# Kernel optimization log

Hardware: AMD Instinct MI355X
Metric: run time of the kernel (lower is better)

The kernel has to match this reference:

```python
import jax, jax.numpy as jnp
import numpy as np

MIN_R, MAX_R = -51.2, 51.2
ORIG_W, ORIG_H = 800.0, 448.0


def sample_bilinear(feat, gx, gy):
    # feat [N,C,H,W]; gx,gy [N,Q] in grid coords [-1,1], align_corners=True, zeros padding
    N, C, H, W = feat.shape
    px = (gx + 1.0) * 0.5 * (W - 1)
    py = (gy + 1.0) * 0.5 * (H - 1)
    x0 = jnp.floor(px)
    y0 = jnp.floor(py)
    x0i = x0.astype(jnp.int32)
    y0i = y0.astype(jnp.int32)
    wx1 = px - x0
    wy1 = py - y0
    ff = feat.reshape(N, C, H * W)

    def corner(xi, yi, w):
        valid = (xi >= 0) & (xi < W) & (yi >= 0) & (yi < H)
        idx = jnp.clip(yi, 0, H - 1) * W + jnp.clip(xi, 0, W - 1)
        vals = jax.vmap(lambda f, i: f[:, i])(ff, idx)  # [N,C,Q]
        return vals * (w * valid.astype(w.dtype))[:, None, :]

    return (corner(x0i, y0i, (1 - wx1) * (1 - wy1))
            + corner(x0i + 1, y0i, wx1 * (1 - wy1))
            + corner(x0i, y0i + 1, (1 - wx1) * wy1)
            + corner(x0i + 1, y0i + 1, wx1 * wy1))


def setup_inputs() -> dict:
    key = jax.random.key(0)
    ks = jax.random.split(key, 16)
    B, Q, C, N = 2, 900, 256, 6
    levels = [(112, 200), (56, 100), (28, 50), (14, 25)]
    inp = {
        'query': jax.random.normal(ks[0], (B, Q, C), jnp.float32),
        'reference_points': jax.random.uniform(ks[1], (B, Q, 3), jnp.float32),
        'key_padding_mask': jax.random.bernoulli(ks[2], 0.1, (B, Q)),
        'cam_intrinsics': jax.random.normal(ks[3], (B, N, 3, 3), jnp.float32),
        'cam_extrinsics': jax.random.normal(ks[4], (B, N, 4, 4), jnp.float32),
    }
    for li, (h, w) in enumerate(levels):
        inp[f'feats_l{li}'] = jax.random.normal(ks[5 + li], (B, N, C, h, w), jnp.float32)
    inp['Wq'] = jax.random.normal(ks[10], (C, C), jnp.float32) * 0.02
    inp['bq'] = jnp.zeros((C,), jnp.float32)
    inp['Wv'] = jax.random.normal(ks[11], (C, C), jnp.float32) * 0.02
    inp['bv'] = jnp.zeros((C,), jnp.float32)
    inp['Wo'] = jax.random.normal(ks[12], (C, C), jnp.float32) * 0.02
    inp['bo'] = jnp.zeros((C,), jnp.float32)
    return inp


def reference(query, reference_points, key_padding_mask, cam_intrinsics, cam_extrinsics,
              feats_l0, feats_l1, feats_l2, feats_l3, Wq, bq, Wv, bv, Wo, bo):
    B, Q, C = query.shape
    N = cam_extrinsics.shape[1]
    mask = key_padding_mask

    ref = reference_points * (MAX_R - MIN_R) + MIN_R
    ref = jnp.where(mask[..., None], jnp.float32(-1000.0), ref)

    q = query @ Wq.T + bq

    ref_hom = jnp.concatenate([ref, jnp.ones((B, Q, 1), ref.dtype)], axis=-1)  # [B,Q,4]
    inv_ext = jnp.nan_to_num(jnp.linalg.inv(cam_extrinsics), nan=0.0, posinf=1e6, neginf=-1e6)
    # per-cam: points_cam_hom = ref_hom @ inv_ext^T  -> [B,N,Q,4]
    pts_cam_hom = jnp.einsum('bqj,bnij->bnqi', ref_hom, inv_ext)
    depth = jnp.nan_to_num(pts_cam_hom[..., 2:3], nan=10.0, posinf=100.0, neginf=-100.0)
    invalid = depth[..., 0] < 1.5  # [B,N,Q]
    depth_safe = jnp.maximum(depth, 1.5)
    pts_cam = pts_cam_hom[..., :3] / depth_safe
    pts_img = jnp.einsum('bnqj,bnij->bnqi', pts_cam, cam_intrinsics)[..., :2]
    pts_img = jnp.clip(pts_img, -3000.0, 3000.0)  # [B,N,Q,2]

    level_sum = jnp.zeros((B * N, C, Q), jnp.float32)
    for feat in (feats_l0, feats_l1, feats_l2, feats_l3):
        Hf, Wf = feat.shape[3], feat.shape[4]
        fx = pts_img[..., 0] * (Wf / ORIG_W)
        fy = pts_img[..., 1] * (Hf / ORIG_H)
        gx = jnp.clip(fx / (Wf - 1.0) * 2.0 - 1.0, -10.0, 10.0)
        gy = jnp.clip(fy / (Hf - 1.0) * 2.0 - 1.0, -10.0, 10.0)
        gx = jnp.where(invalid, jnp.float32(-100.0), gx)
        gy = jnp.where(invalid, jnp.float32(-100.0), gy)
        s = sample_bilinear(feat.reshape(B * N, C, Hf, Wf),
                            gx.reshape(B * N, Q), gy.reshape(B * N, Q))
        level_sum = level_sum + jnp.nan_to_num(s)

    ms = (level_sum / 4.0).reshape(B, N, C, Q).transpose(0, 1, 3, 2)  # [B,N,Q,C]
    v = ms @ Wv.T + bv
    sampled = jnp.max(v, axis=1)  # max over cameras -> [B,Q,C]

    fused = jax.nn.relu(q + sampled) + q
    out = fused @ Wo.T + bo
    out = out * (~mask)[..., None].astype(out.dtype)
    return out
```

## Files before the change

kernel.cpp:

```cpp
#include <hip/hip_runtime.h>
#include <hip/hip_bf16.h>
#include <math.h>

#define BB 2
#define NCAM 6
#define NQ 900
#define NC 256
#define BN (BB*NCAM)
#define NROW (BB*NQ)
#define RPB 2

#define HW0 22400
#define HW1 5600
#define HW2 1400
#define HW3 350

typedef float f4 __attribute__((ext_vector_type(4)));
typedef unsigned short u16x4 __attribute__((ext_vector_type(4)));
typedef struct __attribute__((aligned(4))) { float x, y; } pf2;

__device__ __forceinline__ float u2f(unsigned short u){
  union{unsigned int v; float fl;} x; x.v=((unsigned int)u)<<16; return x.fl;
}

template<int F>
__device__ __forceinline__ float ld1(const void* p, long i){
  if (F) return u2f(((const unsigned short*)p)[i]);
  return ((const float*)p)[i];
}
template<int F>
__device__ __forceinline__ f4 ld4(const void* p, long i){
  if (F){
    u16x4 u = *(const u16x4*)((const unsigned short*)p + i);
    f4 r; r.x=u2f(u.x); r.y=u2f(u.y); r.z=u2f(u.z); r.w=u2f(u.w); return r;
  }
  return *(const f4*)((const float*)p + i);
}

template<int F>
__device__ __forceinline__ void corner4(const void* fp, long cb, int offA, int offB,
                                        int d0, int d1, float* v){
  if (F){
    v[0]=ld1<1>(fp,cb+offA+d0); v[1]=ld1<1>(fp,cb+offA+d1);
    v[2]=ld1<1>(fp,cb+offB+d0); v[3]=ld1<1>(fp,cb+offB+d1);
  } else {
    pf2 a = *(const pf2*)((const float*)fp + cb + offA);
    pf2 b = *(const pf2*)((const float*)fp + cb + offB);
    v[0]=d0?a.y:a.x; v[1]=d1?a.y:a.x;
    v[2]=d0?b.y:b.x; v[3]=d1?b.y:b.x;
  }
}

__device__ __forceinline__ int sniff_flag(const unsigned char* refraw){
  int cnt=0;
  for (int i=1;i<64;i+=4){
    unsigned char b = refraw[i];
    if (b>=0x30 && b<0x40) cnt++;
  }
  return (cnt>=12) ? 1 : 0;
}

#define TILES2 (8*44)
#define TILES3 (8*11)
__global__ __launch_bounds__(256) void prep_all(
    const unsigned char* __restrict__ refraw,
    const void* __restrict__ ext,
    const unsigned char* __restrict__ mask_raw,
    const void* __restrict__ Wq, const void* __restrict__ Wv,
    const void* __restrict__ Wo,
    const void* __restrict__ f2, const void* __restrict__ f3,
    int nW, int nT2t, int nT3t,
    int* __restrict__ flag_out, float* __restrict__ inv_out,
    int* __restrict__ mask_out,
    float* __restrict__ Wblk, float* __restrict__ T2buf,
    float* __restrict__ T3buf){
  __shared__ int sflag, s_na, s_gt, s_bf;
  __shared__ float tile[32][33];
  int t = threadIdx.x;
  int bi = blockIdx.x;
  if (t==0){ sflag = sniff_flag(refraw); s_na=0; s_gt=0; s_bf=0; }
  __syncthreads();
  int f = sflag;

  if (bi < nW){
    int e = bi*256 + t;
    int mat = e >> 16;
    int i = e & 65535;
    int tt = i >> 8, k = i & 255;
    const void* W = (mat==0)?Wq:((mat==1)?Wv:Wo);
    float v = f ? u2f(((const unsigned short*)W)[i]) : ((const float*)W)[i];
    Wblk[mat*65536 + (k>>2)*1024 + tt*4 + (k&3)] = v;
    return;
  }
  if (bi < nW+nT2t+nT3t){
    int idx = bi - nW;
    const void* src; float* dst; int HW, tpb, tp;
    if (idx < nT2t){ HW=HW2; src=f2; dst=T2buf; tpb=TILES2; tp=44; }
    else { idx -= nT2t; HW=HW3; src=f3; dst=T3buf; tpb=TILES3; tp=11; }
    int bn = idx / tpb; int rem = idx - bn*tpb;
    int ct = rem / tp,  pt = rem - ct*tp;
    int c0 = ct*32, p0 = pt*32;
    int ty = t>>5, tx = t&31;
    #pragma unroll
    for (int r=0;r<4;r++){
      int c = c0 + ty + r*8;
      int p = p0 + tx;
      float v = 0.f;
      if (p < HW){
        long s = (long)(bn*NC + c)*HW + p;
        v = f ? u2f(((const unsigned short*)src)[s]) : ((const float*)src)[s];
      }
      tile[ty+r*8][tx] = v;
    }
    __syncthreads();
    #pragma unroll
    for (int r=0;r<4;r++){
      int p = p0 + ty + r*8;
      if (p < HW)
        dst[((long)bn*HW + p)*NC + c0 + tx] = tile[tx][ty+r*8];
    }
    return;
  }

  int f_na=0, f_gt=0, f_bf=0;
  for (int i=t;i<NROW;i+=blockDim.x){
    unsigned char b = mask_raw[i];
    if ((i&3)!=0 && b!=0) f_na=1;
    if (b>1) f_gt=1;
    if ((i&3)==1 && b==0x3f) f_bf=1;
  }
  if (f_na) atomicOr(&s_na,1);
  if (f_gt) atomicOr(&s_gt,1);
  if (f_bf) atomicOr(&s_bf,1);
  __syncthreads();
  int fmt;
  if (!s_na) fmt=0;
  else if (!s_gt) fmt=1;
  else fmt = s_bf ? 2 : 3;
  for (int i=t;i<NROW;i+=blockDim.x){
    int v;
    if (fmt==0)      v = (((const int*)mask_raw)[i]            != 0);
    else if (fmt==1) v = (mask_raw[i]                          != 0);
    else if (fmt==2) v = (((const unsigned short*)mask_raw)[i] != 0);
    else             v = (((const float*)mask_raw)[i]          != 0.0f);
    mask_out[i]=v;
  }
  if (t==0) *flag_out = f;
  if (t < BN){
    double a[4][8];
    for(int i=0;i<4;i++){
      for(int j=0;j<4;j++) a[i][j] = (double)(f? u2f(((const unsigned short*)ext)[t*16+i*4+j])
                                               : ((const float*)ext)[t*16+i*4+j]);
      for(int j=0;j<4;j++) a[i][4+j] = (i==j)?1.0:0.0;
    }
    for(int col=0;col<4;col++){
      int piv=col; double best=fabs(a[col][col]);
      for(int r=col+1;r<4;r++){ double v=fabs(a[r][col]); if(v>best){best=v;piv=r;} }
      if(piv!=col) for(int j=0;j<8;j++){ double tmp=a[col][j]; a[col][j]=a[piv][j]; a[piv][j]=tmp; }
      double id = 1.0/a[col][col];
      for(int j=0;j<8;j++) a[col][j]*=id;
      for(int r=0;r<4;r++) if(r!=col){
        double fc=a[r][col];
        for(int j=0;j<8;j++) a[r][j]-=fc*a[col][j];
      }
    }
    for(int i=0;i<4;i++)for(int j=0;j<4;j++){
      float v=(float)a[i][4+j];
      if (isnan(v)) v=0.f;
      else if (isinf(v)) v = (v>0.f)?1e6f:-1e6f;
      inv_out[t*16+i*4+j]=v;
    }
  }
}

struct SharedMem {
  float q[RPB][NC];
  float ms[RPB][NCAM][NC];
  float fus[RPB][NC];
  float px[RPB][NCAM], py[RPB][NCAM];
  int   iv[RPB][NCAM];
  int   off[RPB][NCAM*4][4];
  float wgt[RPB][NCAM*4][4];
};

template<int F, int RL, int RF>
__device__ __forceinline__ void fused_body(
    const void* __restrict__ query, const void* __restrict__ refpts,
    const void* __restrict__ intr,
    const void* __restrict__ f0, const void* __restrict__ f1,
    const void* __restrict__ f2, const void* __restrict__ f3,
    const void* __restrict__ Wq, const void* __restrict__ bq,
    const void* __restrict__ Wv, const void* __restrict__ bv,
    const void* __restrict__ Wo, const void* __restrict__ bo,
    const float* __restrict__ Wblk,
    const float* __restrict__ T2buf, const float* __restrict__ T3buf,
    const float* __restrict__ inv_ext, const int* __restrict__ mask_int,
    float* __restrict__ out, SharedMem& sm){
  int r0 = blockIdx.x*RPB;
  int t = threadIdx.x;

  const f4* Wq4 = (const f4*)(Wblk);
  const f4* Wv4 = (const f4*)(Wblk + 65536);
  const f4* Wo4 = (const f4*)(Wblk + 131072);

  #pragma unroll
  for(int i=0;i<RPB;i++) sm.q[i][t] = ld1<F>(query,(long)(r0+i)*NC+t);

  if (t < RPB*NCAM){
    int i = t/NCAM, n = t - i*NCAM;
    int row = r0+i, b = row/NQ;
    int m = mask_int[row];
    float h0 = ld1<F>(refpts,(long)row*3+0)*102.4f - 51.2f;
    float h1 = ld1<F>(refpts,(long)row*3+1)*102.4f - 51.2f;
    float h2 = ld1<F>(refpts,(long)row*3+2)*102.4f - 51.2f;
    if (m){ h0=-1000.f; h1=-1000.f; h2=-1000.f; }
    const float* M = inv_ext + (b*NCAM+n)*16;
    float c0 = M[0]*h0 + M[1]*h1 + M[2]*h2 + M[3];
    float c1 = M[4]*h0 + M[5]*h1 + M[6]*h2 + M[7];
    float c2 = M[8]*h0 + M[9]*h1 + M[10]*h2 + M[11];
    float depth = c2;
    if (isnan(depth)) depth = 10.f;
    else if (isinf(depth)) depth = (depth>0)?100.f:-100.f;
    int iv = (depth < 1.5f);
    float ds = fmaxf(depth, 1.5f);
    float pc0=c0/ds, pc1=c1/ds, pc2=c2/ds;
    long kb = (long)(b*NCAM+n)*9;
    float ix = ld1<F>(intr,kb+0)*pc0 + ld1<F>(intr,kb+1)*pc1 + ld1<F>(intr,kb+2)*pc2;
    float iy = ld1<F>(intr,kb+3)*pc0 + ld1<F>(intr,kb+4)*pc1 + ld1<F>(intr,kb+5)*pc2;
    sm.px[i][n] = fminf(fmaxf(ix,-3000.f),3000.f);
    sm.py[i][n] = fminf(fmaxf(iy,-3000.f),3000.f);
    sm.iv[i][n] = iv;
  }
  __syncthreads();

  if (t < RPB*NCAM*4){
    const int Ws_[4]={200,100,50,25}, Hs_[4]={112,56,28,14};
    int i = t/(NCAM*4), u = t - i*(NCAM*4);
    int n = u>>2, l = u&3;
    float x=sm.px[i][n], y=sm.py[i][n];
    int iv=sm.iv[i][n];
    int W=Ws_[l], H=Hs_[l];
    float gx = (x * ((float)W/800.f)) / (W-1.f) * 2.f - 1.f;
    float gy = (y * ((float)H/448.f)) / (H-1.f) * 2.f - 1.f;
    gx=fminf(fmaxf(gx,-10.f),10.f); gy=fminf(fmaxf(gy,-10.f),10.f);
    if(iv){gx=-100.f;gy=-100.f;}
    float pxx=(gx+1.f)*0.5f*(W-1.f);
    float pyy=(gy+1.f)*0.5f*(H-1.f);
    float x0f=floorf(pxx), y0f=floorf(pyy);
    int x0=(int)x0f, y0=(int)y0f;
    float wx1=pxx-x0f, wy1=pyy-y0f, wx0=1.f-wx1, wy0=1.f-wy1;
    int vx0=(x0>=0)&(x0<W), vx1=(x0+1>=0)&(x0+1<W);
    int vy0=(y0>=0)&(y0<H), vy1=(y0+1>=0)&(y0+1<H);
    int cx0=min(max(x0,0),W-1), cx1=min(max(x0+1,0),W-1);
    int cy0=min(max(y0,0),H-1), cy1=min(max(y0+1,0),H-1);
    int px = min(max(x0,0),W-2);
    int d0 = cx0 - px, d1 = cx1 - px;
    sm.off[i][u][0]=cy0*W+px; sm.off[i][u][1]=cy1*W+px;
    sm.off[i][u][2]=d0;       sm.off[i][u][3]=d1;
    sm.wgt[i][u][0]=wx0*wy0*(float)(vx0&vy0);
    sm.wgt[i][u][1]=wx1*wy0*(float)(vx1&vy0);
    sm.wgt[i][u][2]=wx0*wy1*(float)(vx0&vy1);
    sm.wgt[i][u][3]=wx1*wy1*(float)(vx1&vy1);
  }
  __syncthreads();

  {
    #pragma unroll
    for(int n=0;n<NCAM;n++){
      #pragma unroll
      for(int i=0;i<RPB;i++){
        int b = (r0+i)/NQ;
        int bn = b*NCAM+n;
        int chan = bn*NC + t;
        float v[16];
        corner4<F>(f0, (long)chan*HW0,
                   sm.off[i][n*4+0][0], sm.off[i][n*4+0][1],
                   sm.off[i][n*4+0][2], sm.off[i][n*4+0][3], &v[0]);
        corner4<F>(f1, (long)chan*HW1,
                   sm.off[i][n*4+1][0], sm.off[i][n*4+1][1],
                   sm.off[i][n*4+1][2], sm.off[i][n*4+1][3], &v[4]);
        {
          int u=n*4+2;
          if (RF>=2){
            const float* Tp = T2buf + (long)bn*(HW2*NC) + t;
            int oA=sm.off[i][u][0], oB=sm.off[i][u][1], d0=sm.off[i][u][2], d1=sm.off[i][u][3];
            v[8] =Tp[(long)(oA+d0)*NC]; v[9] =Tp[(long)(oA+d1)*NC];
            v[10]=Tp[(long)(oB+d0)*NC]; v[11]=Tp[(long)(oB+d1)*NC];
          } else {
            corner4<F>(f2, (long)chan*HW2,
                       sm.off[i][u][0], sm.off[i][u][1],
                       sm.off[i][u][2], sm.off[i][u][3], &v[8]);
          }
        }
        {
          int u=n*4+3;
          if (RF>=1){
            const float* Tp = T3buf + (long)bn*(HW3*NC) + t;
            int oA=sm.off[i][u][0], oB=sm.off[i][u][1], d0=sm.off[i][u][2], d1=sm.off[i][u][3];
            v[12]=Tp[(long)(oA+d0)*NC]; v[13]=Tp[(long)(oA+d1)*NC];
            v[14]=Tp[(long)(oB+d0)*NC]; v[15]=Tp[(long)(oB+d1)*NC];
          } else {
            corner4<F>(f3, (long)chan*HW3,
                       sm.off[i][u][0], sm.off[i][u][1],
                       sm.off[i][u][2], sm.off[i][u][3], &v[12]);
          }
        }
        float acc=0.f;
        #pragma unroll
        for(int l=0;l<4;l++){
          #pragma unroll
          for(int c=0;c<4;c++)
            acc = fmaf(sm.wgt[i][n*4+l][c], v[l*4+c], acc);
        }
        sm.ms[i][n][t]=acc*0.25f;
      }
    }
  }

  float qv[RPB];
  #pragma unroll
  for(int i=0;i<RPB;i++) qv[i]=0.f;
  {
    #pragma unroll 8
    for(int k4=0;k4<NC/4;k4++){
      f4 wv = RL ? Wq4[k4*256 + t] : ld4<F>(Wq, (long)t*NC + 4*k4);
      #pragma unroll
      for(int i=0;i<RPB;i++){
        f4 xv = ((const f4*)sm.q[i])[k4];
        qv[i]=fmaf(wv.x,xv.x,qv[i]); qv[i]=fmaf(wv.y,xv.y,qv[i]);
        qv[i]=fmaf(wv.z,xv.z,qv[i]); qv[i]=fmaf(wv.w,xv.w,qv[i]);
      }
    }
    float bqv = ld1<F>(bq,t);
    #pragma unroll
    for(int i=0;i<RPB;i++) qv[i]+=bqv;
  }
  __syncthreads();

  float ac[RPB][NCAM];
  #pragma unroll
  for(int i=0;i<RPB;i++)
    #pragma unroll
    for(int n=0;n<NCAM;n++) ac[i][n]=0.f;
  {
    #pragma unroll 2
    for(int k4=0;k4<NC/4;k4++){
      f4 wv = RL ? Wv4[k4*256 + t] : ld4<F>(Wv, (long)t*NC + 4*k4);
      #pragma unroll
      for(int i=0;i<RPB;i++){
        #pragma unroll
        for(int n=0;n<NCAM;n++){
          f4 mv=((const f4*)sm.ms[i][n])[k4];
          ac[i][n]=fmaf(wv.x,mv.x,ac[i][n]); ac[i][n]=fmaf(wv.y,mv.y,ac[i][n]);
          ac[i][n]=fmaf(wv.z,mv.z,ac[i][n]); ac[i][n]=fmaf(wv.w,mv.w,ac[i][n]);
        }
      }
    }
  }
  {
    float bvv = ld1<F>(bv,t);
    #pragma unroll
    for(int i=0;i<RPB;i++){
      float sv = ac[i][0];
      #pragma unroll
      for(int n=1;n<NCAM;n++) sv = fmaxf(sv, ac[i][n]);
      sv += bvv;
      sm.fus[i][t] = fmaxf(qv[i]+sv, 0.f) + qv[i];
    }
  }
  __syncthreads();

  float o[RPB];
  #pragma unroll
  for(int i=0;i<RPB;i++) o[i]=0.f;
  {
    #pragma unroll 8
    for(int k4=0;k4<NC/4;k4++){
      f4 wv = RL ? Wo4[k4*256 + t] : ld4<F>(Wo, (long)t*NC + 4*k4);
      #pragma unroll
      for(int i=0;i<RPB;i++){
        f4 xv = ((const f4*)sm.fus[i])[k4];
        o[i]=fmaf(wv.x,xv.x,o[i]); o[i]=fmaf(wv.y,xv.y,o[i]);
        o[i]=fmaf(wv.z,xv.z,o[i]); o[i]=fmaf(wv.w,xv.w,o[i]);
      }
    }
    float bov = ld1<F>(bo,t);
    #pragma unroll
    for(int i=0;i<RPB;i++){
      int m = mask_int[r0+i];
      float r = o[i] + bov;
      if (m) r = 0.f;
      out[(long)(r0+i)*NC+t] = r;
    }
  }
}

template<int RL, int RF>
__global__ __launch_bounds__(256,4) void fused_kernel(
    const void* query, const void* refpts, const void* intr,
    const void* f0, const void* f1, const void* f2, const void* f3,
    const void* Wq, const void* bq, const void* Wv, const void* bv,
    const void* Wo, const void* bo, const float* __restrict__ Wblk,
    const float* __restrict__ T2buf, const float* __restrict__ T3buf,
    const float* __restrict__ inv_ext, const int* __restrict__ mask_int,
    const int* __restrict__ flag, float* __restrict__ out){
  __shared__ SharedMem sm;
  if (*flag)
    fused_body<1,RL,RF>(query,refpts,intr,f0,f1,f2,f3,Wq,bq,Wv,bv,Wo,bo,
                        Wblk,T2buf,T3buf,inv_ext,mask_int,out,sm);
  else
    fused_body<0,RL,RF>(query,refpts,intr,f0,f1,f2,f3,Wq,bq,Wv,bv,Wo,bo,
                        Wblk,T2buf,T3buf,inv_ext,mask_int,out,sm);
}

extern "C" void kernel_launch(void* const* d_in, const int* in_sizes, int n_in,
                              void* d_out, int out_size, void* d_ws, size_t ws_size,
                              hipStream_t stream){
  const void* query  = d_in[0];
  const void* refpts = d_in[1];
  const unsigned char* mask_raw = (const unsigned char*)d_in[2];
  const void* intr   = d_in[3];
  const void* ext    = d_in[4];
  const void* f0     = d_in[5];
  const void* f1     = d_in[6];
  const void* f2     = d_in[7];
  const void* f3     = d_in[8];
  const void* Wq     = d_in[9];
  const void* bq     = d_in[10];
  const void* Wv     = d_in[11];
  const void* bv     = d_in[12];
  const void* Wo     = d_in[13];
  const void* bo     = d_in[14];

  char* ws = (char*)d_ws;
  float* inv_ext  = (float*)(ws + 0);
  int*   dflag    = (int*)  (ws + 1024);
  int*   mask_int = (int*)  (ws + 2048);
  float* Wblk     = (float*)(ws + 16384);
  float* T3buf    = (float*)(ws + 802816);
  float* T2buf    = (float*)(ws + 5103616);

  const size_t needW  = 802816;
  const size_t need3  = 5103616;
  const size_t need23 = 22306816;

  int rl = (ws_size >= needW) ? 1 : 0;
  int rf = (ws_size >= need23) ? 2 : ((ws_size >= need3) ? 1 : 0);

  int nW   = rl ? 768 : 0;
  int nT2t = (rf>=2) ? BN*TILES2 : 0;
  int nT3t = (rf>=1) ? BN*TILES3 : 0;

  hipLaunchKernelGGL(prep_all, dim3(nW+nT2t+nT3t+1), dim3(256), 0, stream,
                     (const unsigned char*)refpts, ext, mask_raw,
                     Wq, Wv, Wo, f2, f3, nW, nT2t, nT3t,
                     dflag, inv_ext, mask_int, Wblk, T2buf, T3buf);

  dim3 grid(NROW/RPB);
  if (rl && rf==2)
    hipLaunchKernelGGL(HIP_KERNEL_NAME(fused_kernel<1,2>), grid, dim3(256), 0, stream,
                       query, refpts, intr, f0, f1, f2, f3,
                       Wq, bq, Wv, bv, Wo, bo, Wblk, T2buf, T3buf,
                       inv_ext, mask_int, dflag, (float*)d_out);
  else if (rl && rf==1)
    hipLaunchKernelGGL(HIP_KERNEL_NAME(fused_kernel<1,1>), grid, dim3(256), 0, stream,
                       query, refpts, intr, f0, f1, f2, f3,
                       Wq, bq, Wv, bv, Wo, bo, Wblk, T2buf, T3buf,
                       inv_ext, mask_int, dflag, (float*)d_out);
  else if (rl)
    hipLaunchKernelGGL(HIP_KERNEL_NAME(fused_kernel<1,0>), grid, dim3(256), 0, stream,
                       query, refpts, intr, f0, f1, f2, f3,
                       Wq, bq, Wv, bv, Wo, bo, Wblk, T2buf, T3buf,
                       inv_ext, mask_int, dflag, (float*)d_out);
  else
    hipLaunchKernelGGL(HIP_KERNEL_NAME(fused_kernel<0,0>), grid, dim3(256), 0, stream,
                       query, refpts, intr, f0, f1, f2, f3,
                       Wq, bq, Wv, bv, Wo, bo, Wblk, T2buf, T3buf,
                       inv_ext, mask_int, dflag, (float*)d_out);
}
```

Baseline: 494.3 us.

## Split fused kernel into sampling kernel and query-tiled projection tail kernel

Replaces the single fused sample-plus-projection kernel with two kernels. A per-row sampling kernel writes the camera-level averaged features to a workspace buffer, and a tail kernel then handles four queries per block for the Wq/Wv/Wo projections. This increases weight reuse per block in the matmuls and shrinks the sampling kernel's footprint, at the cost of an extra launch and a round trip of roughly 11 MB of intermediates through global memory. The fallback path drops the transposed-weight and transposed-level options when the workspace is too small.

Result: no change. 496.4 us (+0.4%).

```diff
diff --git a/kernel.cpp b/kernel.cpp
--- a/kernel.cpp
+++ b/kernel.cpp
@@ -9,6 +9,7 @@
 #define BN (BB*NCAM)
 #define NROW (BB*NQ)
 #define RPB 2
+#define QT 4
 
 #define HW0 22400
 #define HW1 5600
@@ -173,6 +174,243 @@
   }
 }
 
+struct SampleSM {
+  float px[NCAM], py[NCAM];
+  int   iv[NCAM];
+  int   off[NCAM*4][4];
+  float wgt[NCAM*4][4];
+};
+
+template<int F>
+__device__ __forceinline__ void sample_body(
+    const void* __restrict__ refpts, const void* __restrict__ intr,
+    const void* __restrict__ f0, const void* __restrict__ f1,
+    const float* __restrict__ T2buf, const float* __restrict__ T3buf,
+    const float* __restrict__ inv_ext, const int* __restrict__ mask_int,
+    float* __restrict__ Sbuf, SampleSM& sm){
+  int row = blockIdx.x;
+  int b = row/NQ;
+  int q = row - b*NQ;
+  int t = threadIdx.x;
+  int m = mask_int[row];
+
+  if (t < NCAM){
+    float h0 = ld1<F>(refpts,(long)row*3+0)*102.4f - 51.2f;
+    float h1 = ld1<F>(refpts,(long)row*3+1)*102.4f - 51.2f;
+    float h2 = ld1<F>(refpts,(long)row*3+2)*102.4f - 51.2f;
+    if (m){ h0=-1000.f; h1=-1000.f; h2=-1000.f; }
+    const float* M = inv_ext + (b*NCAM+t)*16;
+    float c0 = M[0]*h0 + M[1]*h1 + M[2]*h2 + M[3];
+    float c1 = M[4]*h0 + M[5]*h1 + M[6]*h2 + M[7];
+    float c2 = M[8]*h0 + M[9]*h1 + M[10]*h2 + M[11];
+    float depth = c2;
+    if (isnan(depth)) depth = 10.f;
+    else if (isinf(depth)) depth = (depth>0)?100.f:-100.f;
+    int iv = (depth < 1.5f);
+    float ds = fmaxf(depth, 1.5f);
+    float pc0=c0/ds, pc1=c1/ds, pc2=c2/ds;
+    long kb = (long)(b*NCAM+t)*9;
+    float ix = ld1<F>(intr,kb+0)*pc0 + ld1<F>(intr,kb+1)*pc1 + ld1<F>(intr,kb+2)*pc2;
+    float iy = ld1<F>(intr,kb+3)*pc0 + ld1<F>(intr,kb+4)*pc1 + ld1<F>(intr,kb+5)*pc2;
+    sm.px[t] = fminf(fmaxf(ix,-3000.f),3000.f);
+    sm.py[t] = fminf(fmaxf(iy,-3000.f),3000.f);
+    sm.iv[t] = iv;
+  }
+  __syncthreads();
+
+  if (t < NCAM*4){
+    const int Ws_[4]={200,100,50,25}, Hs_[4]={112,56,28,14};
+    int n=t>>2, l=t&3;
+    float x=sm.px[n], y=sm.py[n];
+    int iv=sm.iv[n];
+    int W=Ws_[l], H=Hs_[l];
+    float gx = (x * ((float)W/800.f)) / (W-1.f) * 2.f - 1.f;
+    float gy = (y * ((float)H/448.f)) / (H-1.f) * 2.f - 1.f;
+    gx=fminf(fmaxf(gx,-10.f),10.f); gy=fminf(fmaxf(gy,-10.f),10.f);
+    if(iv){gx=-100.f;gy=-100.f;}
+    float pxx=(gx+1.f)*0.5f*(W-1.f);
+    float pyy=(gy+1.f)*0.5f*(H-1.f);
+    float x0f=floorf(pxx), y0f=floorf(pyy);
+    int x0=(int)x0f, y0=(int)y0f;
+    float wx1=pxx-x0f, wy1=pyy-y0f, wx0=1.f-wx1, wy0=1.f-wy1;
+    int vx0=(x0>=0)&(x0<W), vx1=(x0+1>=0)&(x0+1<W);
+    int vy0=(y0>=0)&(y0<H), vy1=(y0+1>=0)&(y0+1<H);
+    int cx0=min(max(x0,0),W-1), cx1=min(max(x0+1,0),W-1);
+    int cy0=min(max(y0,0),H-1), cy1=min(max(y0+1,0),H-1);
+    int px = min(max(x0,0),W-2);
+    int d0 = cx0 - px, d1 = cx1 - px;
+    sm.off[t][0]=cy0*W+px; sm.off[t][1]=cy1*W+px;
+    sm.off[t][2]=d0;       sm.off[t][3]=d1;
+    sm.wgt[t][0]=wx0*wy0*(float)(vx0&vy0);
+    sm.wgt[t][1]=wx1*wy0*(float)(vx1&vy0);
+    sm.wgt[t][2]=wx0*wy1*(float)(vx0&vy1);
+    sm.wgt[t][3]=wx1*wy1*(float)(vx1&vy1);
+  }
+  __syncthreads();
+
+  int bnb = b*NCAM;
+  #pragma unroll
+  for(int n=0;n<NCAM;n++){
+    int bn = bnb+n;
+    int chan = bn*NC + t;
+    float v[16];
+    corner4<F>(f0, (long)chan*HW0,
+               sm.off[n*4+0][0], sm.off[n*4+0][1],
+               sm.off[n*4+0][2], sm.off[n*4+0][3], &v[0]);
+    corner4<F>(f1, (long)chan*HW1,
+               sm.off[n*4+1][0], sm.off[n*4+1][1],
+               sm.off[n*4+1][2], sm.off[n*4+1][3], &v[4]);
+    {
+      int u=n*4+2;
+      const float* Tp = T2buf + (long)bn*(HW2*NC) + t;
+      int oA=sm.off[u][0], oB=sm.off[u][1], d0=sm.off[u][2], d1=sm.off[u][3];
+      v[8] =Tp[(long)(oA+d0)*NC]; v[9] =Tp[(long)(oA+d1)*NC];
+      v[10]=Tp[(long)(oB+d0)*NC]; v[11]=Tp[(long)(oB+d1)*NC];
+    }
+    {
+      int u=n*4+3;
+      const float* Tp = T3buf + (long)bn*(HW3*NC) + t;
+      int oA=sm.off[u][0], oB=sm.off[u][1], d0=sm.off[u][2], d1=sm.off[u][3];
+      v[12]=Tp[(long)(oA+d0)*NC]; v[13]=Tp[(long)(oA+d1)*NC];
+      v[14]=Tp[(long)(oB+d0)*NC]; v[15]=Tp[(long)(oB+d1)*NC];
+    }
+    float acc=0.f;
+    #pragma unroll
+    for(int l=0;l<4;l++){
+      #pragma unroll
+      for(int c=0;c<4;c++)
+        acc = fmaf(sm.wgt[n*4+l][c], v[l*4+c], acc);
+    }
+    Sbuf[((long)bn*NQ + q)*NC + t] = acc*0.25f;
+  }
+}
+
+__global__ __launch_bounds__(256,4) void sample_kernel(
+    const void* refpts, const void* intr,
+    const void* f0, const void* f1,
+    const float* __restrict__ T2buf, const float* __restrict__ T3buf,
+    const float* __restrict__ inv_ext, const int* __restrict__ mask_int,
+    const int* __restrict__ flag, float* __restrict__ Sbuf){
+  __shared__ SampleSM sm;
+  if (*flag) sample_body<1>(refpts,intr,f0,f1,T2buf,T3buf,inv_ext,mask_int,Sbuf,sm);
+  else       sample_body<0>(refpts,intr,f0,f1,T2buf,T3buf,inv_ext,mask_int,Sbuf,sm);
+}
+
+template<int F>
+__device__ __forceinline__ void tail_body(
+    const void* __restrict__ query,
+    const void* __restrict__ bq, const void* __restrict__ bv,
+    const void* __restrict__ bo,
+    const float* __restrict__ Wblk, const float* __restrict__ Sbuf,
+    const int* __restrict__ mask_int, float* __restrict__ out,
+    float (*sq)[NC], float (*sms)[QT][NC], float (*fus)[NC]){
+  int bi = blockIdx.x;
+  int b  = bi / (NQ/QT);
+  int q0 = (bi - b*(NQ/QT)) * QT;
+  int t  = threadIdx.x;
+
+  const f4* Wq4 = (const f4*)(Wblk);
+  const f4* Wv4 = (const f4*)(Wblk + 65536);
+  const f4* Wo4 = (const f4*)(Wblk + 131072);
+
+  #pragma unroll
+  for (int r=0;r<QT;r++)
+    sq[r][t] = ld1<F>(query, (long)(b*NQ+q0+r)*NC + t);
+  #pragma unroll
+  for (int n=0;n<NCAM;n++)
+    #pragma unroll
+    for (int r=0;r<QT;r++)
+      sms[n][r][t] = Sbuf[((long)(b*NCAM+n)*NQ + q0+r)*NC + t];
+  __syncthreads();
+
+  float qv[QT];
+  #pragma unroll
+  for (int r=0;r<QT;r++) qv[r]=0.f;
+  #pragma unroll 4
+  for (int k4=0;k4<NC/4;k4++){
+    f4 wv = Wq4[k4*256 + t];
+    #pragma unroll
+    for (int r=0;r<QT;r++){
+      f4 xv = ((const f4*)sq[r])[k4];
+      qv[r]=fmaf(wv.x,xv.x,qv[r]); qv[r]=fmaf(wv.y,xv.y,qv[r]);
+      qv[r]=fmaf(wv.z,xv.z,qv[r]); qv[r]=fmaf(wv.w,xv.w,qv[r]);
+    }
+  }
+  {
+    float bqv = ld1<F>(bq,t);
+    #pragma unroll
+    for (int r=0;r<QT;r++) qv[r]+=bqv;
+  }
+
+  float av[NCAM][QT];
+  #pragma unroll
+  for (int n=0;n<NCAM;n++)
+    #pragma unroll
+    for (int r=0;r<QT;r++) av[n][r]=0.f;
+  #pragma unroll 2
+  for (int k4=0;k4<NC/4;k4++){
+    f4 wv = Wv4[k4*256 + t];
+    #pragma unroll
+    for (int n=0;n<NCAM;n++){
+      #pragma unroll
+      for (int r=0;r<QT;r++){
+        f4 mv = ((const f4*)sms[n][r])[k4];
+        av[n][r]=fmaf(wv.x,mv.x,av[n][r]); av[n][r]=fmaf(wv.y,mv.y,av[n][r]);
+        av[n][r]=fmaf(wv.z,mv.z,av[n][r]); av[n][r]=fmaf(wv.w,mv.w,av[n][r]);
+      }
+    }
+  }
+  {
+    float bvv = ld1<F>(bv,t);
+    #pragma unroll
+    for (int r=0;r<QT;r++){
+      float sv = av[0][r];
+      #pragma unroll
+      for (int n=1;n<NCAM;n++) sv = fmaxf(sv, av[n][r]);
+      sv += bvv;
+      fus[r][t] = fmaxf(qv[r]+sv, 0.f) + qv[r];
+    }
+  }
+  __syncthreads();
+
+  float o[QT];
+  #pragma unroll
+  for (int r=0;r<QT;r++) o[r]=0.f;
+  #pragma unroll 4
+  for (int k4=0;k4<NC/4;k4++){
+    f4 wv = Wo4[k4*256 + t];
+    #pragma unroll
+    for (int r=0;r<QT;r++){
+      f4 xv = ((const f4*)fus[r])[k4];
+      o[r]=fmaf(wv.x,xv.x,o[r]); o[r]=fmaf(wv.y,xv.y,o[r]);
+      o[r]=fmaf(wv.z,xv.z,o[r]); o[r]=fmaf(wv.w,xv.w,o[r]);
+    }
+  }
+  {
+    float bov = ld1<F>(bo,t);
+    #pragma unroll
+    for (int r=0;r<QT;r++){
+      int row = b*NQ+q0+r;
+      int m = mask_int[row];
+      float rr = o[r] + bov;
+      if (m) rr = 0.f;
+      out[(long)row*NC+t] = rr;
+    }
+  }
+}
+
+__global__ __launch_bounds__(256,2) void tail_kernel(
+    const void* query, const void* bq, const void* bv, const void* bo,
+    const float* __restrict__ Wblk, const float* __restrict__ Sbuf,
+    const int* __restrict__ mask_int, const int* __restrict__ flag,
+    float* __restrict__ out){
+  __shared__ __align__(16) float sq[QT][NC];
+  __shared__ __align__(16) float sms[NCAM][QT][NC];
+  __shared__ __align__(16) float fus[QT][NC];
+  if (*flag) tail_body<1>(query,bq,bv,bo,Wblk,Sbuf,mask_int,out,sq,sms,fus);
+  else       tail_body<0>(query,bq,bv,bo,Wblk,Sbuf,mask_int,out,sq,sms,fus);
+}
+
 struct SharedMem {
   float q[RPB][NC];
   float ms[RPB][NCAM][NC];
@@ -183,7 +421,7 @@
   float wgt[RPB][NCAM*4][4];
 };
 
-template<int F, int RL, int RF>
+template<int F>
 __device__ __forceinline__ void fused_body(
     const void* __restrict__ query, const void* __restrict__ refpts,
     const void* __restrict__ intr,
@@ -192,16 +430,10 @@
     const void* __restrict__ Wq, const void* __restrict__ bq,
     const void* __restrict__ Wv, const void* __restrict__ bv,
     const void* __restrict__ Wo, const void* __restrict__ bo,
-    const float* __restrict__ Wblk,
-    const float* __restrict__ T2buf, const float* __restrict__ T3buf,
     const float* __restrict__ inv_ext, const int* __restrict__ mask_int,
     float* __restrict__ out, SharedMem& sm){
   int r0 = blockIdx.x*RPB;
   int t = threadIdx.x;
-
-  const f4* Wq4 = (const f4*)(Wblk);
-  const f4* Wv4 = (const f4*)(Wblk + 65536);
-  const f4* Wo4 = (const f4*)(Wblk + 131072);
 
   #pragma unroll
   for(int i=0;i<RPB;i++) sm.q[i][t] = ld1<F>(query,(long)(r0+i)*NC+t);
@@ -265,53 +497,28 @@
   __syncthreads();
 
   {
+    const long HWs[4]={HW0,HW1,HW2,HW3};
+    const void* fb[4]={f0,f1,f2,f3};
     #pragma unroll
     for(int n=0;n<NCAM;n++){
       #pragma unroll
       for(int i=0;i<RPB;i++){
         int b = (r0+i)/NQ;
-        int bn = b*NCAM+n;
-        int chan = bn*NC + t;
+        int chan = (b*NCAM+n)*NC + t;
         float v[16];
-        corner4<F>(f0, (long)chan*HW0,
-                   sm.off[i][n*4+0][0], sm.off[i][n*4+0][1],
-                   sm.off[i][n*4+0][2], sm.off[i][n*4+0][3], &v[0]);
-        corner4<F>(f1, (long)chan*HW1,
-                   sm.off[i][n*4+1][0], sm.off[i][n*4+1][1],
-                   sm.off[i][n*4+1][2], sm.off[i][n*4+1][3], &v[4]);
-        {
-          int u=n*4+2;
-          if (RF>=2){
-            const float* Tp = T2buf + (long)bn*(HW2*NC) + t;
-            int oA=sm.off[i][u][0], oB=sm.off[i][u][1], d0=sm.off[i][u][2], d1=sm.off[i][u][3];
-            v[8] =Tp[(long)(oA+d0)*NC]; v[9] =Tp[(long)(oA+d1)*NC];
-            v[10]=Tp[(long)(oB+d0)*NC]; v[11]=Tp[(long)(oB+d1)*NC];
-          } else {
-            corner4<F>(f2, (long)chan*HW2,
-                       sm.off[i][u][0], sm.off[i][u][1],
-                       sm.off[i][u][2], sm.off[i][u][3], &v[8]);
-          }
-        }
-        {
-          int u=n*4+3;
-          if (RF>=1){
-            const float* Tp = T3buf + (long)bn*(HW3*NC) + t;
-            int oA=sm.off[i][u][0], oB=sm.off[i][u][1], d0=sm.off[i][u][2], d1=sm.off[i][u][3];
-            v[12]=Tp[(long)(oA+d0)*NC]; v[13]=Tp[(long)(oA+d1)*NC];
-            v[14]=Tp[(long)(oB+d0)*NC]; v[15]=Tp[(long)(oB+d1)*NC];
-          } else {
-            corner4<F>(f3, (long)chan*HW3,
-                       sm.off[i][u][0], sm.off[i][u][1],
-                       sm.off[i][u][2], sm.off[i][u][3], &v[12]);
-          }
+        #pragma unroll
+        for(int l=0;l<4;l++){
+          int u=n*4+l;
+          corner4<F>(fb[l], (long)chan*HWs[l],
+                     sm.off[i][u][0], sm.off[i][u][1],
+                     sm.off[i][u][2], sm.off[i][u][3], &v[l*4]);
         }
         float acc=0.f;
         #pragma unroll
-        for(int l=0;l<4;l++){
+        for(int l=0;l<4;l++)
           #pragma unroll
           for(int c=0;c<4;c++)
             acc = fmaf(sm.wgt[i][n*4+l][c], v[l*4+c], acc);
-        }
         sm.ms[i][n][t]=acc*0.25f;
       }
     }
@@ -323,7 +530,7 @@
   {
     #pragma unroll 8
     for(int k4=0;k4<NC/4;k4++){
-      f4 wv = RL ? Wq4[k4*256 + t] : ld4<F>(Wq, (long)t*NC + 4*k4);
+      f4 wv = ld4<F>(Wq, (long)t*NC + 4*k4);
       #pragma unroll
       for(int i=0;i<RPB;i++){
         f4 xv = ((const f4*)sm.q[i])[k4];
@@ -345,7 +552,7 @@
   {
     #pragma unroll 2
     for(int k4=0;k4<NC/4;k4++){
-      f4 wv = RL ? Wv4[k4*256 + t] : ld4<F>(Wv, (long)t*NC + 4*k4);
+      f4 wv = ld4<F>(Wv, (long)t*NC + 4*k4);
       #pragma unroll
       for(int i=0;i<RPB;i++){
         #pragma unroll
@@ -376,7 +583,7 @@
   {
     #pragma unroll 8
     for(int k4=0;k4<NC/4;k4++){
-      f4 wv = RL ? Wo4[k4*256 + t] : ld4<F>(Wo, (long)t*NC + 4*k4);
+      f4 wv = ld4<F>(Wo, (long)t*NC + 4*k4);
       #pragma unroll
       for(int i=0;i<RPB;i++){
         f4 xv = ((const f4*)sm.fus[i])[k4];
@@ -395,22 +602,20 @@
   }
 }
 
-template<int RL, int RF>
-__global__ __launch_bounds__(256,4) void fused_kernel(
+__global__ __launch_bounds__(256,4) void fused_kernel_fb(
     const void* query, const void* refpts, const void* intr,
     const void* f0, const void* f1, const void* f2, const void* f3,
     const void* Wq, const void* bq, const void* Wv, const void* bv,
-    const void* Wo, const void* bo, const float* __restrict__ Wblk,
-    const float* __restrict__ T2buf, const float* __restrict__ T3buf,
+    const void* Wo, const void* bo,
     const float* __restrict__ inv_ext, const int* __restrict__ mask_int,
     const int* __restrict__ flag, float* __restrict__ out){
   __shared__ SharedMem sm;
   if (*flag)
-    fused_body<1,RL,RF>(query,refpts,intr,f0,f1,f2,f3,Wq,bq,Wv,bv,Wo,bo,
-                        Wblk,T2buf,T3buf,inv_ext,mask_int,out,sm);
+    fused_body<1>(query,refpts,intr,f0,f1,f2,f3,Wq,bq,Wv,bv,Wo,bo,
+                  inv_ext,mask_int,out,sm);
   else
-    fused_body<0,RL,RF>(query,refpts,intr,f0,f1,f2,f3,Wq,bq,Wv,bv,Wo,bo,
-                        Wblk,T2buf,T3buf,inv_ext,mask_int,out,sm);
+    fused_body<0>(query,refpts,intr,f0,f1,f2,f3,Wq,bq,Wv,bv,Wo,bo,
+                  inv_ext,mask_int,out,sm);
 }
 
 extern "C" void kernel_launch(void* const* d_in, const int* in_sizes, int n_in,
@@ -439,42 +644,32 @@
   float* Wblk     = (float*)(ws + 16384);
   float* T3buf    = (float*)(ws + 802816);
   float* T2buf    = (float*)(ws + 5103616);
-
-  const size_t needW  = 802816;
-  const size_t need3  = 5103616;
-  const size_t need23 = 22306816;
-
-  int rl = (ws_size >= needW) ? 1 : 0;
-  int rf = (ws_size >= need23) ? 2 : ((ws_size >= need3) ? 1 : 0);
-
-  int nW   = rl ? 768 : 0;
-  int nT2t = (rf>=2) ? BN*TILES2 : 0;
-  int nT3t = (rf>=1) ? BN*TILES3 : 0;
-
-  hipLaunchKernelGGL(prep_all, dim3(nW+nT2t+nT3t+1), dim3(256), 0, stream,
-                     (const unsigned char*)refpts, ext, mask_raw,
-                     Wq, Wv, Wo, f2, f3, nW, nT2t, nT3t,
-                     dflag, inv_ext, mask_int, Wblk, T2buf, T3buf);
-
-  dim3 grid(NROW/RPB);
-  if (rl && rf==2)
-    hipLaunchKernelGGL(HIP_KERNEL_NAME(fused_kernel<1,2>), grid, dim3(256), 0, stream,
+  float* Sbuf     = (float*)(ws + 22306816);
+
+  const size_t need_all = 33366016;
+
+  if (ws_size >= need_all){
+    int nW   = 768;
+    int nT2t = BN*TILES2;
+    int nT3t = BN*TILES3;
+    hipLaunchKernelGGL(prep_all, dim3(nW+nT2t+nT3t+1), dim3(256), 0, stream,
+                       (const unsigned char*)refpts, ext, mask_raw,
+                       Wq, Wv, Wo, f2, f3, nW, nT2t, nT3t,
+                       dflag, inv_ext, mask_int, Wblk, T2buf, T3buf);
+    hipLaunchKernelGGL(sample_kernel, dim3(NROW), dim3(256), 0, stream,
+                       refpts, intr, f0, f1, T2buf, T3buf,
+                       inv_ext, mask_int, dflag, Sbuf);
+    hipLaunchKernelGGL(tail_kernel, dim3(BB*(NQ/QT)), dim3(256), 0, stream,
+                       query, bq, bv, bo, Wblk, Sbuf, mask_int, dflag,
+                       (float*)d_out);
+  } else {
+    hipLaunchKernelGGL(prep_all, dim3(1), dim3(256), 0, stream,
+                       (const unsigned char*)refpts, ext, mask_raw,
+                       Wq, Wv, Wo, f2, f3, 0, 0, 0,
+                       dflag, inv_ext, mask_int, Wblk, T2buf, T3buf);
+    hipLaunchKernelGGL(fused_kernel_fb, dim3(NROW/RPB), dim3(256), 0, stream,
                        query, refpts, intr, f0, f1, f2, f3,
-                       Wq, bq, Wv, bv, Wo, bo, Wblk, T2buf, T3buf,
+                       Wq, bq, Wv, bv, Wo, bo,
                        inv_ext, mask_int, dflag, (float*)d_out);
-  else if (rl && rf==1)
-    hipLaunchKernelGGL(HIP_KERNEL_NAME(fused_kernel<1,1>), grid, dim3(256), 0, stream,
-                       query, refpts, intr, f0, f1, f2, f3,
-                       Wq, bq, Wv, bv, Wo, bo, Wblk, T2buf, T3buf,
-                       inv_ext, mask_int, dflag, (float*)d_out);
-  else if (rl)
-    hipLaunchKernelGGL(HIP_KERNEL_NAME(fused_kernel<1,0>), grid, dim3(256), 0, stream,
-                       query, refpts, intr, f0, f1, f2, f3,
-                       Wq, bq, Wv, bv, Wo, bo, Wblk, T2buf, T3buf,
-                       inv_ext, mask_int, dflag, (float*)d_out);
-  else
-    hipLaunchKernelGGL(HIP_KERNEL_NAME(fused_kernel<0,0>), grid, dim3(256), 0, stream,
-                       query, refpts, intr, f0, f1, f2, f3,
-                       Wq, bq, Wv, bv, Wo, bo, Wblk, T2buf, T3buf,
-                       inv_ext, mask_int, dflag, (float*)d_out);
-}
+  }
+}
```
